# Optimization experiments

Hardware: AMD Instinct MI355X
Metric: run time of the kernel (lower is better)

## Reference

```python
import jax, jax.numpy as jnp
import numpy as np

IMAGE_SIZE = 64                 # Rasterize(image_size=64, anti_aliasing=True)
RASTER = IMAGE_SIZE * 2 * 2     # init doubles for AA, forward doubles again -> 256
CHUNK = 64
B, NV, NF = 4, 1024, 1024


def setup_inputs() -> dict:
    key = jax.random.key(0)
    k1, k2 = jax.random.split(key)
    vertices = jax.random.uniform(k1, (B, NV, 2), dtype=jnp.float32, minval=-1.0, maxval=1.0)
    faces = jax.random.randint(k2, (B, NF, 3), 0, NV, dtype=jnp.int32)
    return {"vertices": vertices, "faces": faces}


def _pixel_grid(s):
    # NMR-style pixel centers in NDC: p = (2i + 1 - s) / s
    c = (2.0 * jnp.arange(s, dtype=jnp.float32) + 1.0 - s) / s
    py, px = jnp.meshgrid(c, c, indexing="ij")
    return px.reshape(-1), py.reshape(-1)  # (P,), (P,)


def _hard_raster(face_xy, s):
    # face_xy: (B, Nf, 3, 2). Coverage = any face whose 3 edge cross products are all > 0.
    # Faces are duplicated with reversed winding upstream, so a one-sided test covers
    # every non-degenerate triangle regardless of orientation.
    px, py = _pixel_grid(s)
    b, nft = face_xy.shape[:2]
    chunks = face_xy.reshape(b, nft // CHUNK, CHUNK, 3, 2).transpose(1, 0, 2, 3, 4)

    def step(cov, fc):
        v = fc                              # (B, C, 3, 2)
        vn = jnp.roll(v, -1, axis=2)        # next vertex per edge
        ex = (vn[..., 0] - v[..., 0])[..., None]   # (B, C, 3, 1)
        ey = (vn[..., 1] - v[..., 1])[..., None]
        cross = ex * (py - v[..., 1][..., None]) - ey * (px - v[..., 0][..., None])  # (B,C,3,P)
        inside = jnp.all(cross > 0, axis=2)        # (B, C, P)
        return jnp.logical_or(cov, jnp.any(inside, axis=1)), None

    cov0 = jnp.zeros((b, s * s), dtype=bool)
    cov, _ = jax.lax.scan(step, cov0, chunks)
    return cov.astype(jnp.float32).reshape(b, s, s)


def reference(vertices, faces):
    # forward: double faces with reversed winding, gather vertex coords per face
    faces2 = jnp.concatenate([faces, faces[:, :, ::-1]], axis=1)         # (B, 2Nf, 3)
    face_xy = jax.vmap(lambda v, f: v[f])(vertices, faces2)              # (B, 2Nf, 3, 2)
    alpha = _hard_raster(face_xy, RASTER)                                # (B, RASTER, RASTER)
    alpha = alpha[:, ::-1, :]                                            # vertical flip
    b, s, _ = alpha.shape
    alpha = alpha.reshape(b, s // 2, 2, s // 2, 2).mean(axis=(2, 4))     # avg_pool2d k=2
    return alpha
```

## Files before the change

kernel.cpp:

```cpp
#include <hip/hip_runtime.h>


constexpr int S     = 256;
constexpr int NVERT = 1024;
constexpr int NFACE = 1024;
constexpr int OUTSZ = 128;

__global__ __launch_bounds__(256)
void face_setup(const float* __restrict__ verts, const int* __restrict__ faces,
                float4* __restrict__ recs, int total)
{
    const int g = blockIdx.x * 256 + threadIdx.x;
    if (g >= total) return;
    const int b = g >> 10;
    const float* __restrict__ vb = verts + (size_t)b * NVERT * 2;
    const int*   __restrict__ fp = faces + (size_t)g * 3;
    const int i0 = fp[0], i1 = fp[1], i2 = fp[2];
    const float xa = vb[i0 * 2 + 0], ya = vb[i0 * 2 + 1];
    const float xb = vb[i1 * 2 + 0], yb = vb[i1 * 2 + 1];
    const float xc = vb[i2 * 2 + 0], yc = vb[i2 * 2 + 1];
    recs[0 * total + g] = make_float4(xa, ya, xb, yb);
    recs[1 * total + g] = make_float4(xc, yc, __fsub_rn(xb, xa), __fsub_rn(yb, ya));
    recs[2 * total + g] = make_float4(__fsub_rn(xc, xb), __fsub_rn(yc, yb),
                                      __fsub_rn(xa, xc), __fsub_rn(ya, yc));
}

__global__ __launch_bounds__(64)
void raster8(const float4* __restrict__ recs, float* __restrict__ out, int total)
{
    __shared__ float4 fd[64][3];

    const int b   = blockIdx.z;
    const int tid = threadIdx.x;
    const int tx  = tid & 7;
    const int ty  = tid >> 3;
    const int bx  = (int)(blockIdx.x << 3);
    const int by  = (int)(blockIdx.y << 3);
    const int sx  = bx + tx;
    const int sy  = by + ty;

    const float px = (float)(2 * sx + 1 - S) * (1.0f / (float)S);
    const float py = (float)(2 * sy + 1 - S) * (1.0f / (float)S);
    const float rx0 = (float)(2 * bx + 1 - S)       * (1.0f / (float)S);
    const float rx1 = (float)(2 * (bx + 7) + 1 - S) * (1.0f / (float)S);
    const float ry0 = (float)(2 * by + 1 - S)       * (1.0f / (float)S);
    const float ry1 = (float)(2 * (by + 7) + 1 - S) * (1.0f / (float)S);
    constexpr float MARGIN = 1e-4f;
    const float cx = (rx0 + rx1) * 0.5f;
    const float cy = (ry0 + ry1) * 0.5f;
    const float h  = (rx1 - rx0) * 0.5f;
    const float rx0m = rx0 - MARGIN, rx1m = rx1 + MARGIN;
    const float ry0m = ry0 - MARGIN, ry1m = ry1 + MARGIN;

    const float4* __restrict__ P0 = recs + 0 * (size_t)total + (size_t)b * NFACE;
    const float4* __restrict__ P1 = recs + 1 * (size_t)total + (size_t)b * NFACE;
    const float4* __restrict__ P2 = recs + 2 * (size_t)total + (size_t)b * NFACE;

    bool covered = false;

    float4 r0 = P0[tid], r1 = P1[tid], r2 = P2[tid];

    for (int c0 = 0; c0 < NFACE; c0 += 64) {
        const int nidx = ((c0 + 64) & (NFACE - 1)) + tid;
        const float4 n0 = P0[nidx];
        const float4 n1 = P1[nidx];
        const float4 n2 = P2[nidx];

        bool keep;
        {
            const float xa = r0.x, ya = r0.y, xb = r0.z, yb = r0.w;
            const float xc = r1.x, yc = r1.y;
            const float exab = r1.z, eyab = r1.w;
            const float exbc = r2.x, eybc = r2.y;
            const float exca = r2.z, eyca = r2.w;
            const float xmn = fminf(xa, fminf(xb, xc));
            const float xmx = fmaxf(xa, fmaxf(xb, xc));
            const float ymn = fminf(ya, fminf(yb, yc));
            const float ymx = fmaxf(ya, fmaxf(yb, yc));
            const bool bbok = (xmn <= rx1m) & (xmx >= rx0m) &
                              (ymn <= ry1m) & (ymx >= ry0m);
            #define EDGE_CR(ex, ey, vx, vy, Fc, rr)                           \
                const float Fc = (ex) * (cy - (vy)) - (ey) * (cx - (vx));     \
                const float rr = (fabsf(ex) + fabsf(ey)) * h;
            EDGE_CR(exab, eyab, xa, ya, FcAB, rAB)
            EDGE_CR(exbc, eybc, xb, yb, FcBC, rBC)
            EDGE_CR(exca, eyca, xc, yc, FcCA, rCA)
            #undef EDGE_CR
            const bool fwdPossible = (FcAB + rAB > -MARGIN) &
                                     (FcBC + rBC > -MARGIN) &
                                     (FcCA + rCA > -MARGIN);
            const bool revPossible = (FcAB - rAB <  MARGIN) &
                                     (FcBC - rBC <  MARGIN) &
                                     (FcCA - rCA <  MARGIN);
            keep = bbok & (fwdPossible | revPossible);
        }

        const unsigned long long m = __ballot((int)keep);
        const int cnt = __popcll(m);
        if (keep) {
            const int slot = __popcll(m & ((1ull << tid) - 1));
            fd[slot][0] = r0;
            fd[slot][1] = r1;
            fd[slot][2] = r2;
        }
        __syncthreads();

        for (int i = 0; i < cnt; ++i) {
            const float4 A  = fd[i][0];
            const float4 Bv = fd[i][1];
            const float4 C  = fd[i][2];
            const float dxa = __fsub_rn(px, A.x),  dya = __fsub_rn(py, A.y);
            const float dxb = __fsub_rn(px, A.z),  dyb = __fsub_rn(py, A.w);
            const float dxc = __fsub_rn(px, Bv.x), dyc = __fsub_rn(py, Bv.y);
            const float exab = Bv.z, eyab = Bv.w;
            const float exbc = C.x,  eybc = C.y;
            const float exca = C.z,  eyca = C.w;
            const float F0 = __fsub_rn(__fmul_rn(exab, dya), __fmul_rn(eyab, dxa));
            const float F1 = __fsub_rn(__fmul_rn(exbc, dyb), __fmul_rn(eybc, dxb));
            const float F2 = __fsub_rn(__fmul_rn(exca, dyc), __fmul_rn(eyca, dxc));
            const float R0 = __fsub_rn(__fmul_rn(eybc, dxc), __fmul_rn(exbc, dyc));
            const float R1 = __fsub_rn(__fmul_rn(eyab, dxb), __fmul_rn(exab, dyb));
            const float R2 = __fsub_rn(__fmul_rn(eyca, dxa), __fmul_rn(exca, dya));
            const bool fwd = (F0 > 0.0f) & (F1 > 0.0f) & (F2 > 0.0f);
            const bool rev = (R0 > 0.0f) & (R1 > 0.0f) & (R2 > 0.0f);
            covered = covered || fwd || rev;
            if (__all((int)covered)) break;
        }

        const bool done = __all((int)covered);
        __syncthreads();
        if (done) break;
        r0 = n0; r1 = n1; r2 = n2;
    }

    float c = covered ? 1.0f : 0.0f;
    c += __shfl_xor(c, 1);
    c += __shfl_xor(c, 8);
    if (((tx & 1) == 0) && ((ty & 1) == 0)) {
        const int X = sx >> 1;
        const int Y = (OUTSZ - 1) - (sy >> 1);
        out[((size_t)b * OUTSZ + Y) * OUTSZ + X] = c * 0.25f;
    }
}

extern "C" void kernel_launch(void* const* d_in, const int* in_sizes, int n_in,
                              void* d_out, int out_size, void* d_ws, size_t ws_size,
                              hipStream_t stream) {
    const float* verts = (const float*)d_in[0];
    const int*   faces = (const int*)d_in[1];
    float*       out   = (float*)d_out;

    const int B     = in_sizes[0] / (NVERT * 2);
    const int total = B * NFACE;

    float4* recs = (float4*)d_ws;

    face_setup<<<(total + 255) / 256, 256, 0, stream>>>(verts, faces, recs, total);

    dim3 grid(S / 8, S / 8, B);
    raster8<<<grid, dim3(64), 0, stream>>>(recs, out, total);
}
```

Measured before the change: 24.06 us.

## Fuse face setup into raster kernel with four waves splitting faces per tile

Drops the separate face-setup kernel. Each raster block now loads its batch's vertices into LDS and gathers face vertices itself through the face indices. Blocks grow to four waves, each handling a disjoint quarter of the faces for the same 8x8 pixel tile. The waves share coverage through an LDS atomicOr mask so all can exit early, and block barriers in the loop are replaced by per-wave LDS waits. This removes a launch and the global intermediate buffer, at the cost of a per-block vertex load (8KB) and redundant edge setup in every tile block.

Measured after the change: 19.62 us. -18.5%, faster.

```diff
diff --git a/kernel.cpp b/kernel.cpp
--- a/kernel.cpp
+++ b/kernel.cpp
@@ -7,40 +7,27 @@
 constexpr int OUTSZ = 128;
 
 __global__ __launch_bounds__(256)
-void face_setup(const float* __restrict__ verts, const int* __restrict__ faces,
-                float4* __restrict__ recs, int total)
+void raster_fused(const float* __restrict__ verts,
+                  const int*   __restrict__ faces,
+                  float*       __restrict__ out)
 {
-    const int g = blockIdx.x * 256 + threadIdx.x;
-    if (g >= total) return;
-    const int b = g >> 10;
-    const float* __restrict__ vb = verts + (size_t)b * NVERT * 2;
-    const int*   __restrict__ fp = faces + (size_t)g * 3;
-    const int i0 = fp[0], i1 = fp[1], i2 = fp[2];
-    const float xa = vb[i0 * 2 + 0], ya = vb[i0 * 2 + 1];
-    const float xb = vb[i1 * 2 + 0], yb = vb[i1 * 2 + 1];
-    const float xc = vb[i2 * 2 + 0], yc = vb[i2 * 2 + 1];
-    recs[0 * total + g] = make_float4(xa, ya, xb, yb);
-    recs[1 * total + g] = make_float4(xc, yc, __fsub_rn(xb, xa), __fsub_rn(yb, ya));
-    recs[2 * total + g] = make_float4(__fsub_rn(xc, xb), __fsub_rn(yc, yb),
-                                      __fsub_rn(xa, xc), __fsub_rn(ya, yc));
-}
+    __shared__ float2 vlds[NVERT];
+    __shared__ float4 fd[4][64][3];
+    __shared__ unsigned long long covMask;
 
-__global__ __launch_bounds__(64)
-void raster8(const float4* __restrict__ recs, float* __restrict__ out, int total)
-{
-    __shared__ float4 fd[64][3];
+    const int b    = blockIdx.z;
+    const int tid  = threadIdx.x;
+    const int lane = tid & 63;
+    const int wid  = tid >> 6;
+    const int tx   = lane & 7;
+    const int ty   = lane >> 3;
+    const int bx   = (int)(blockIdx.x << 3);
+    const int by   = (int)(blockIdx.y << 3);
+    const int sx   = bx + tx;
+    const int sy   = by + ty;
 
-    const int b   = blockIdx.z;
-    const int tid = threadIdx.x;
-    const int tx  = tid & 7;
-    const int ty  = tid >> 3;
-    const int bx  = (int)(blockIdx.x << 3);
-    const int by  = (int)(blockIdx.y << 3);
-    const int sx  = bx + tx;
-    const int sy  = by + ty;
-
-    const float px = (float)(2 * sx + 1 - S) * (1.0f / (float)S);
-    const float py = (float)(2 * sy + 1 - S) * (1.0f / (float)S);
+    const float px  = (float)(2 * sx + 1 - S)       * (1.0f / (float)S);
+    const float py  = (float)(2 * sy + 1 - S)       * (1.0f / (float)S);
     const float rx0 = (float)(2 * bx + 1 - S)       * (1.0f / (float)S);
     const float rx1 = (float)(2 * (bx + 7) + 1 - S) * (1.0f / (float)S);
     const float ry0 = (float)(2 * by + 1 - S)       * (1.0f / (float)S);
@@ -52,27 +39,44 @@
     const float rx0m = rx0 - MARGIN, rx1m = rx1 + MARGIN;
     const float ry0m = ry0 - MARGIN, ry1m = ry1 + MARGIN;
 
-    const float4* __restrict__ P0 = recs + 0 * (size_t)total + (size_t)b * NFACE;
-    const float4* __restrict__ P1 = recs + 1 * (size_t)total + (size_t)b * NFACE;
-    const float4* __restrict__ P2 = recs + 2 * (size_t)total + (size_t)b * NFACE;
+    {
+        const float4* __restrict__ v4 = (const float4*)(verts + (size_t)b * NVERT * 2);
+        float4* __restrict__ l4 = (float4*)vlds;
+        #pragma unroll
+        for (int i = 0; i < NVERT / 2 / 256; ++i)
+            l4[tid + i * 256] = v4[tid + i * 256];
+    }
+    if (tid == 0) covMask = 0ull;
+    __syncthreads();
+
+    const int* __restrict__ fb = faces + (size_t)b * NFACE * 3;
 
     bool covered = false;
 
-    float4 r0 = P0[tid], r1 = P1[tid], r2 = P2[tid];
+    int c0 = wid * 64;
+    int i0 = fb[3 * (c0 + lane) + 0];
+    int i1 = fb[3 * (c0 + lane) + 1];
+    int i2 = fb[3 * (c0 + lane) + 2];
 
-    for (int c0 = 0; c0 < NFACE; c0 += 64) {
-        const int nidx = ((c0 + 64) & (NFACE - 1)) + tid;
-        const float4 n0 = P0[nidx];
-        const float4 n1 = P1[nidx];
-        const float4 n2 = P2[nidx];
+    for (; c0 < NFACE; c0 += 256) {
+        const int nc = c0 + 256;
+        int n0 = 0, n1 = 0, n2 = 0;
+        if (nc < NFACE) {
+            n0 = fb[3 * (nc + lane) + 0];
+            n1 = fb[3 * (nc + lane) + 1];
+            n2 = fb[3 * (nc + lane) + 2];
+        }
+
+        const float2 va = vlds[i0], vbb = vlds[i1], vcc = vlds[i2];
+        const float xa = va.x,  ya = va.y;
+        const float xb = vbb.x, yb = vbb.y;
+        const float xc = vcc.x, yc = vcc.y;
+        const float exab = __fsub_rn(xb, xa), eyab = __fsub_rn(yb, ya);
+        const float exbc = __fsub_rn(xc, xb), eybc = __fsub_rn(yc, yb);
+        const float exca = __fsub_rn(xa, xc), eyca = __fsub_rn(ya, yc);
 
         bool keep;
         {
-            const float xa = r0.x, ya = r0.y, xb = r0.z, yb = r0.w;
-            const float xc = r1.x, yc = r1.y;
-            const float exab = r1.z, eyab = r1.w;
-            const float exbc = r2.x, eybc = r2.y;
-            const float exca = r2.z, eyca = r2.w;
             const float xmn = fminf(xa, fminf(xb, xc));
             const float xmx = fmaxf(xa, fmaxf(xb, xc));
             const float ymn = fminf(ya, fminf(yb, yc));
@@ -86,60 +90,68 @@
             EDGE_CR(exbc, eybc, xb, yb, FcBC, rBC)
             EDGE_CR(exca, eyca, xc, yc, FcCA, rCA)
             #undef EDGE_CR
-            const bool fwdPossible = (FcAB + rAB > -MARGIN) &
-                                     (FcBC + rBC > -MARGIN) &
-                                     (FcCA + rCA > -MARGIN);
-            const bool revPossible = (FcAB - rAB <  MARGIN) &
-                                     (FcBC - rBC <  MARGIN) &
-                                     (FcCA - rCA <  MARGIN);
-            keep = bbok & (fwdPossible | revPossible);
+            const bool fwdP = (FcAB + rAB > -MARGIN) & (FcBC + rBC > -MARGIN) &
+                              (FcCA + rCA > -MARGIN);
+            const bool revP = (FcAB - rAB <  MARGIN) & (FcBC - rBC <  MARGIN) &
+                              (FcCA - rCA <  MARGIN);
+            keep = bbok & (fwdP | revP);
         }
 
         const unsigned long long m = __ballot((int)keep);
         const int cnt = __popcll(m);
+        asm volatile("s_waitcnt lgkmcnt(0)" ::: "memory");
         if (keep) {
-            const int slot = __popcll(m & ((1ull << tid) - 1));
-            fd[slot][0] = r0;
-            fd[slot][1] = r1;
-            fd[slot][2] = r2;
+            const int slot = __popcll(m & ((1ull << lane) - 1));
+            fd[wid][slot][0] = make_float4(xa, ya, xb, yb);
+            fd[wid][slot][1] = make_float4(xc, yc, exab, eyab);
+            fd[wid][slot][2] = make_float4(exbc, eybc, exca, eyca);
         }
-        __syncthreads();
+        asm volatile("s_waitcnt lgkmcnt(0)" ::: "memory");
 
         for (int i = 0; i < cnt; ++i) {
-            const float4 A  = fd[i][0];
-            const float4 Bv = fd[i][1];
-            const float4 C  = fd[i][2];
+            const float4 A  = fd[wid][i][0];
+            const float4 Bv = fd[wid][i][1];
+            const float4 C  = fd[wid][i][2];
             const float dxa = __fsub_rn(px, A.x),  dya = __fsub_rn(py, A.y);
             const float dxb = __fsub_rn(px, A.z),  dyb = __fsub_rn(py, A.w);
             const float dxc = __fsub_rn(px, Bv.x), dyc = __fsub_rn(py, Bv.y);
-            const float exab = Bv.z, eyab = Bv.w;
-            const float exbc = C.x,  eybc = C.y;
-            const float exca = C.z,  eyca = C.w;
-            const float F0 = __fsub_rn(__fmul_rn(exab, dya), __fmul_rn(eyab, dxa));
-            const float F1 = __fsub_rn(__fmul_rn(exbc, dyb), __fmul_rn(eybc, dxb));
-            const float F2 = __fsub_rn(__fmul_rn(exca, dyc), __fmul_rn(eyca, dxc));
-            const float R0 = __fsub_rn(__fmul_rn(eybc, dxc), __fmul_rn(exbc, dyc));
-            const float R1 = __fsub_rn(__fmul_rn(eyab, dxb), __fmul_rn(exab, dyb));
-            const float R2 = __fsub_rn(__fmul_rn(eyca, dxa), __fmul_rn(exca, dya));
+            const float e0x = Bv.z, e0y = Bv.w;
+            const float e1x = C.x,  e1y = C.y;
+            const float e2x = C.z,  e2y = C.w;
+            const float F0 = __fsub_rn(__fmul_rn(e0x, dya), __fmul_rn(e0y, dxa));
+            const float F1 = __fsub_rn(__fmul_rn(e1x, dyb), __fmul_rn(e1y, dxb));
+            const float F2 = __fsub_rn(__fmul_rn(e2x, dyc), __fmul_rn(e2y, dxc));
+            const float R0 = __fsub_rn(__fmul_rn(e1y, dxc), __fmul_rn(e1x, dyc));
+            const float R1 = __fsub_rn(__fmul_rn(e0y, dxb), __fmul_rn(e0x, dyb));
+            const float R2 = __fsub_rn(__fmul_rn(e2y, dxa), __fmul_rn(e2x, dya));
             const bool fwd = (F0 > 0.0f) & (F1 > 0.0f) & (F2 > 0.0f);
             const bool rev = (R0 > 0.0f) & (R1 > 0.0f) & (R2 > 0.0f);
             covered = covered || fwd || rev;
             if (__all((int)covered)) break;
         }
 
-        const bool done = __all((int)covered);
-        __syncthreads();
-        if (done) break;
-        r0 = n0; r1 = n1; r2 = n2;
+        const unsigned long long m2 = __ballot((int)covered);
+        unsigned long long u = 0ull;
+        if (lane == 0) u = atomicOr(&covMask, m2) | m2;
+        u = __shfl(u, 0);
+        if (u == ~0ull) break;
+
+        i0 = n0; i1 = n1; i2 = n2;
     }
 
-    float c = covered ? 1.0f : 0.0f;
-    c += __shfl_xor(c, 1);
-    c += __shfl_xor(c, 8);
-    if (((tx & 1) == 0) && ((ty & 1) == 0)) {
-        const int X = sx >> 1;
-        const int Y = (OUTSZ - 1) - (sy >> 1);
-        out[((size_t)b * OUTSZ + Y) * OUTSZ + X] = c * 0.25f;
+    __syncthreads();
+
+    if (tid < 64) {
+        const unsigned long long u = covMask;
+        if (((tx & 1) == 0) && ((ty & 1) == 0)) {
+            const float c = (float)(((u >> lane) & 1ull) +
+                                    ((u >> (lane ^ 1)) & 1ull) +
+                                    ((u >> (lane ^ 8)) & 1ull) +
+                                    ((u >> (lane ^ 9)) & 1ull));
+            const int X = sx >> 1;
+            const int Y = (OUTSZ - 1) - (sy >> 1);
+            out[((size_t)b * OUTSZ + Y) * OUTSZ + X] = c * 0.25f;
+        }
     }
 }
 
@@ -150,13 +162,7 @@
     const int*   faces = (const int*)d_in[1];
     float*       out   = (float*)d_out;
 
-    const int B     = in_sizes[0] / (NVERT * 2);
-    const int total = B * NFACE;
-
-    float4* recs = (float4*)d_ws;
-
-    face_setup<<<(total + 255) / 256, 256, 0, stream>>>(verts, faces, recs, total);
-
+    const int B = in_sizes[0] / (NVERT * 2);
     dim3 grid(S / 8, S / 8, B);
-    raster8<<<grid, dim3(64), 0, stream>>>(recs, out, total);
+    raster_fused<<<grid, dim3(256), 0, stream>>>(verts, faces, out);
 }
```
